# Performance work log

Measured on AMD Instinct MI355X. Metric: run time of the kernel, lower is better.

Reference implementation:

```python
import jax, jax.numpy as jnp
import numpy as np

V, H, B, NS, SL, QL, AL = 100000, 256, 64, 40, 30, 20, 12
NUM_EPISODE = 3


def setup_inputs() -> dict:
    key = jax.random.key(0)
    ks = iter(jax.random.split(key, 48))
    def p(shape, scale=0.05):
        return jax.random.normal(next(ks), shape, jnp.float32) * scale
    d = {}
    d["c_p"] = jax.random.randint(next(ks), (B, NS, SL), 0, V, dtype=jnp.int32)
    d["c_mask"] = jnp.zeros((B, NS, SL), jnp.int32)
    d["q_p"] = jax.random.randint(next(ks), (B, QL), 0, V, dtype=jnp.int32)
    d["q_mask"] = jnp.zeros((B, QL), jnp.int32)
    d["a_I_p"] = jax.random.randint(next(ks), (B, AL), 0, V, dtype=jnp.int32)
    d["a_I_mask"] = jnp.zeros((B, AL), jnp.int32)
    d["a_II_p"] = jax.random.randint(next(ks), (B, AL), 0, V, dtype=jnp.int32)
    d["a_II_mask"] = jnp.zeros((B, AL), jnp.int32)
    d["embed"] = p((V, H)).at[0].set(0.0)  # padding_idx=0
    for name in ["ctx", "q", "ans", "attn", "mem"]:
        d[name + "_Wih"] = p((3 * H, H))
        d[name + "_Whh"] = p((3 * H, H))
        d[name + "_bih"] = p((3 * H,))
        d[name + "_bhh"] = p((3 * H,))
    d["gate_W1"] = p((H, 7 * H)); d["gate_b1"] = p((H,))
    d["gate_W2"] = p((1, H));     d["gate_b2"] = p((1,))
    d["out_W1"] = p((H, 3 * H)); d["out_b1"] = p((H,))
    d["out_W2"] = p((2, H));     d["out_b2"] = p((2,))
    return d


def _gru_step(h, gi_t, Whh, bhh):
    # PyTorch GRU cell math; gates ordered (r, z, n)
    gh = h @ Whh.T + bhh
    i_r, i_z, i_n = jnp.split(gi_t, 3, -1)
    h_r, h_z, h_n = jnp.split(gh, 3, -1)
    r = jax.nn.sigmoid(i_r + h_r)
    z = jax.nn.sigmoid(i_z + h_z)
    n = jnp.tanh(i_n + r * h_n)
    return (1.0 - z) * n + z * h


def _run_gru(x, Wih, Whh, bih, bhh):
    # x: [N, T, H] -> outputs [N, T, H], zero initial hidden
    gi = jnp.einsum('nth,gh->ntg', x, Wih) + bih  # precompute input projections
    h0 = jnp.zeros((x.shape[0], Whh.shape[1]), x.dtype)
    def step(h, g_t):
        h2 = _gru_step(h, g_t, Whh, bhh)
        return h2, h2
    _, outs = jax.lax.scan(step, h0, jnp.swapaxes(gi, 0, 1))
    return jnp.swapaxes(outs, 0, 1)


def _gather_last(outs, mask):
    # real_length = number of zeros in mask (0 marks a valid token)
    lengths = jnp.sum(mask == 0, axis=-1)
    idx = jnp.clip(lengths - 1, 0, outs.shape[1] - 1)
    return jnp.take_along_axis(outs, idx[:, None, None], axis=1)[:, 0]


def _forward(c_p, c_mask, q_p, q_mask, a_I_p, a_I_mask, a_II_p, a_II_mask,
             embed,
             ctx_Wih, ctx_Whh, ctx_bih, ctx_bhh,
             q_Wih, q_Whh, q_bih, q_bhh,
             ans_Wih, ans_Whh, ans_bih, ans_bhh,
             attn_Wih, attn_Whh, attn_bih, attn_bhh,
             mem_Wih, mem_Whh, mem_bih, mem_bhh,
             gate_W1, gate_b1, gate_W2, gate_b2,
             out_W1, out_b1, out_W2, out_b2):
    b, ns, sl = c_p.shape
    # Context encoding: all (batch, sentence) pairs through one batched GRU
    ce = embed[c_p.reshape(b * ns, sl)]                      # [B*NS, SL, H]
    c_out = _run_gru(ce, ctx_Wih, ctx_Whh, ctx_bih, ctx_bhh)
    enc_ctx = _gather_last(c_out, c_mask.reshape(b * ns, sl)).reshape(b, ns, -1)  # [B, NS, H]
    # Question / answers
    enc_q = _gather_last(_run_gru(embed[q_p], q_Wih, q_Whh, q_bih, q_bhh), q_mask)          # [B, H]
    enc_a1 = _gather_last(_run_gru(embed[a_I_p], ans_Wih, ans_Whh, ans_bih, ans_bhh), a_I_mask)
    enc_a2 = _gather_last(_run_gru(embed[a_II_p], ans_Wih, ans_Whh, ans_bih, ans_bhh), a_II_mask)
    # Episodic memory: gated attention GRU scan over context sentences
    ctx_t = jnp.swapaxes(enc_ctx, 0, 1)  # [NS, B, H]
    memory = enc_q
    for _ in range(NUM_EPISODE):
        mem_now = memory
        def step(h, ct):
            feat = jnp.concatenate([ct, mem_now, enc_q, ct * enc_q, ct * mem_now,
                                    jnp.abs(ct - enc_q), jnp.abs(ct - mem_now)], axis=1)  # [B, 7H]
            g = jax.nn.sigmoid(jnp.tanh(feat @ gate_W1.T + gate_b1) @ gate_W2.T + gate_b2)  # [B, 1]
            hc = _gru_step(h, ct @ attn_Wih.T + attn_bih, attn_Whh, attn_bhh)
            return g * hc + (1.0 - g) * h, None
        e, _ = jax.lax.scan(step, jnp.zeros_like(memory), ctx_t)
        memory = _gru_step(memory, e @ mem_Wih.T + mem_bih, mem_Whh, mem_bhh)
    final = jnp.concatenate([memory, enc_a1, enc_a2], axis=1)  # [B, 3H]
    logits = jnp.tanh(final @ out_W1.T + out_b1) @ out_W2.T + out_b2  # [B, 2]
    return jax.nn.softmax(logits, axis=-1)


def reference(c_p, c_mask, q_p, q_mask, a_I_p, a_I_mask, a_II_p, a_II_mask,
              embed,
              ctx_Wih, ctx_Whh, ctx_bih, ctx_bhh,
              q_Wih, q_Whh, q_bih, q_bhh,
              ans_Wih, ans_Whh, ans_bih, ans_bhh,
              attn_Wih, attn_Whh, attn_bih, attn_bhh,
              mem_Wih, mem_Whh, mem_bih, mem_bhh,
              gate_W1, gate_b1, gate_W2, gate_b2,
              out_W1, out_b1, out_W2, out_b2):
    return _forward(c_p, c_mask, q_p, q_mask, a_I_p, a_I_mask, a_II_p, a_II_mask,
                    embed,
                    ctx_Wih, ctx_Whh, ctx_bih, ctx_bhh,
                    q_Wih, q_Whh, q_bih, q_bhh,
                    ans_Wih, ans_Whh, ans_bih, ans_bhh,
                    attn_Wih, attn_Whh, attn_bih, attn_bhh,
                    mem_Wih, mem_Whh, mem_bih, mem_bhh,
                    gate_W1, gate_b1, gate_W2, gate_b2,
                    out_W1, out_b1, out_W2, out_b2)
```

## Files before the change

kernel.cpp:

```cpp
#include <hip/hip_runtime.h>

typedef unsigned short u16;
typedef __bf16 bf16x8 __attribute__((ext_vector_type(8)));
typedef float f32x4 __attribute__((ext_vector_type(4)));

#define NSENT 40
#define SLEN 30
#define QLEN 20
#define ALEN 12
#define SCTX 2560

__device__ __forceinline__ float b2f(u16 u){ union{float f; unsigned i;} v; v.i = ((unsigned)u)<<16; return v.f; }
__device__ __forceinline__ u16 f2b(float f){ union{float f; unsigned u;} v; v.f=f; unsigned u=v.u; u += ((u>>16)&1u) + 0x7fffu; return (u16)(u>>16); }
__device__ __forceinline__ float sigm(float x){ return __builtin_amdgcn_rcpf(1.f + __expf(-x)); }
__device__ __forceinline__ float tanh_(float x){
  float a = fminf(fmaxf(2.f*x, -30.f), 30.f);
  float e = __expf(a);
  return 1.f - 2.f*__builtin_amdgcn_rcpf(e + 1.f);
}
__device__ __forceinline__ f32x4 mfma16(bf16x8 a, bf16x8 b, f32x4 c){
  return __builtin_amdgcn_mfma_f32_16x16x32_bf16(a, b, c, 0, 0, 0);
}

__global__ void k_prep(
    const float* s0,const float* s1,const float* s2,const float* s3,const float* s4,
    const float* s5,const float* s6,const float* s7,const float* s8,const float* s9,
    const float* s10,
    u16* d0,u16* d1,u16* d2,u16* d3,u16* d4,u16* d5,u16* d6,u16* d7,u16* d8,u16* d9,u16* d10)
{
  int i = blockIdx.x*512 + threadIdx.x;
  const float* s; u16* d; int off;
  if (i < 1966080){
    int seg = i/196608; off = i - seg*196608;
    switch(seg){
      case 0: s=s0; d=d0; break;  case 1: s=s1; d=d1; break;
      case 2: s=s2; d=d2; break;  case 3: s=s3; d=d3; break;
      case 4: s=s4; d=d4; break;  case 5: s=s5; d=d5; break;
      case 6: s=s6; d=d6; break;  case 7: s=s7; d=d7; break;
      case 8: s=s8; d=d8; break;  default: s=s9; d=d9; break;
    }
  } else { s=s10; d=d10; off = i - 1966080; }
  d[off] = f2b(s[off]);
}

__global__ __launch_bounds__(512, 2) void k_xproj(
    const int* c_p, const int* q_p, const int* a1p, const int* a2p,
    const float* embed,
    const u16* cWihB, const u16* qWihB, const u16* aWihB,
    const float* cbih, const float* qbih, const float* abih,
    u16* gi_c, u16* gi_q, u16* gi_a1, u16* gi_a2)
{
  __shared__ u16 xb[32][264];
  __shared__ u16 go[32][776];
  int bid=blockIdx.x, tid=threadIdx.x;
  const int* toks; const u16* W; const float* bias; u16* out; int rl;
  if (bid < 2400){ toks=c_p; W=cWihB; bias=cbih; out=gi_c; rl=bid*32; }
  else if (bid < 2440){ toks=q_p; W=qWihB; bias=qbih; out=gi_q; rl=(bid-2400)*32; }
  else if (bid < 2464){ toks=a1p; W=aWihB; bias=abih; out=gi_a1; rl=(bid-2440)*32; }
  else               { toks=a2p; W=aWihB; bias=abih; out=gi_a2; rl=(bid-2464)*32; }
  #pragma unroll
  for (int p=0;p<4;p++){
    int i=p*512+tid; int row=i>>6, f4=i&63;
    int tok = toks[rl+row];
    float4 v = *((const float4*)(embed + (long)tok*256) + f4);
    u16* dst = &xb[row][f4*4];
    dst[0]=f2b(v.x); dst[1]=f2b(v.y); dst[2]=f2b(v.z); dst[3]=f2b(v.w);
  }
  const int w=tid>>6, lane=tid&63, c=lane&15, quad=lane>>4;
  f32x4 acc[2][6];
  #pragma unroll
  for (int Mt=0;Mt<2;Mt++)
    #pragma unroll
    for (int nt=0;nt<6;nt++) acc[Mt][nt]=(f32x4){0.f,0.f,0.f,0.f};
  __syncthreads();
  #pragma unroll
  for (int Kt=0;Kt<8;Kt++){
    bf16x8 a0 = *(const bf16x8*)&xb[c][Kt*32+quad*8];
    bf16x8 a1 = *(const bf16x8*)&xb[16+c][Kt*32+quad*8];
    #pragma unroll
    for (int nt=0;nt<6;nt++){
      bf16x8 bfr = *(const bf16x8*)(W + ((w*6+nt)*16+c)*256 + Kt*32 + quad*8);
      acc[0][nt]=mfma16(a0,bfr,acc[0][nt]);
      acc[1][nt]=mfma16(a1,bfr,acc[1][nt]);
    }
  }
  float biasv[6];
  #pragma unroll
  for (int nt=0;nt<6;nt++) biasv[nt]=bias[(w*6+nt)*16+c];
  #pragma unroll
  for (int Mt=0;Mt<2;Mt++)
    #pragma unroll
    for (int nt=0;nt<6;nt++)
      #pragma unroll
      for (int r=0;r<4;r++)
        go[Mt*16+quad*4+r][(w*6+nt)*16+c]=f2b(acc[Mt][nt][r]+biasv[nt]);
  __syncthreads();
  #pragma unroll
  for (int p=0;p<6;p++){
    int idx=p*512+tid;
    int row=idx/96, ch=idx-row*96;
    *(uint4*)(out + (long)(rl+row)*768 + ch*8) = *(uint4*)((char*)&go[row][0] + ch*16);
  }
}

__global__ __launch_bounds__(512, 2) void k_enc_scan(
    const int* c_mask, const int* q_mask, const int* a1m, const int* a2m,
    const u16* cWhhB, const u16* qWhhB, const u16* aWhhB,
    const float* cbhh, const float* qbhh, const float* abhh,
    const u16* gi_c, const u16* gi_q, const u16* gi_a1, const u16* gi_a2,
    u16* enc_hi, u16* enc_lo, float* enc_qf, float* enc_a1f, float* enc_a2f)
{
  __shared__ u16 hhi[16][264];
  __shared__ u16 hlo[16][264];
  __shared__ float gh[16][772];
  __shared__ float holdf[16][256];
  __shared__ float bhl[768];
  __shared__ int idxs[16];
  int bid=blockIdx.x, tid=threadIdx.x;
  const int* msk; const u16* W; const float* bhh; const u16* gi; int T, seq0, mode;
  u16 *ohi=0, *olo=0; float* of=0;
  if (bid<160){ msk=c_mask; W=cWhhB; bhh=cbhh; gi=gi_c; T=SLEN; seq0=bid*16; mode=0; ohi=enc_hi; olo=enc_lo; }
  else if (bid<164){ msk=q_mask; W=qWhhB; bhh=qbhh; gi=gi_q; T=QLEN; seq0=(bid-160)*16; mode=1; of=enc_qf; }
  else if (bid<168){ msk=a1m; W=aWhhB; bhh=abhh; gi=gi_a1; T=ALEN; seq0=(bid-164)*16; mode=1; of=enc_a1f; }
  else             { msk=a2m; W=aWhhB; bhh=abhh; gi=gi_a2; T=ALEN; seq0=(bid-168)*16; mode=1; of=enc_a2f; }
  if (tid<16){
    int len=0; const int* mr=msk+(seq0+tid)*T;
    for (int t=0;t<T;t++) len += (mr[t]==0);
    int id=len-1; if(id<0)id=0; if(id>T-1)id=T-1; idxs[tid]=id;
  }
  for (int i=tid;i<16*264;i+=512){ ((u16*)hhi)[i]=0; ((u16*)hlo)[i]=0; }
  for (int i=tid;i<16*256;i+=512) ((float*)holdf)[i]=0.f;
  for (int i=tid;i<768;i+=512) bhl[i]=bhh[i];
  const int w=tid>>6, lane=tid&63, c=lane&15, quad=lane>>4;
  uint4 breg[48];
  #pragma unroll
  for (int nt=0;nt<6;nt++)
    #pragma unroll
    for (int Kt=0;Kt<8;Kt++)
      breg[nt*8+Kt] = *(const uint4*)(W + ((w*6+nt)*16+c)*256 + Kt*32 + quad*8);
  __syncthreads();

  for (int t=0;t<T;t++){
    f32x4 acc[6];
    #pragma unroll
    for (int nt=0;nt<6;nt++) acc[nt]=(f32x4){0.f,0.f,0.f,0.f};
    #pragma unroll
    for (int Kt=0;Kt<8;Kt++){
      bf16x8 a=*(const bf16x8*)&hhi[c][Kt*32+quad*8];
      #pragma unroll
      for (int nt=0;nt<6;nt++) acc[nt]=mfma16(a,*(const bf16x8*)&breg[nt*8+Kt],acc[nt]);
    }
    #pragma unroll
    for (int Kt=0;Kt<8;Kt++){
      bf16x8 a=*(const bf16x8*)&hlo[c][Kt*32+quad*8];
      #pragma unroll
      for (int nt=0;nt<6;nt++) acc[nt]=mfma16(a,*(const bf16x8*)&breg[nt*8+Kt],acc[nt]);
    }
    #pragma unroll
    for (int nt=0;nt<6;nt++)
      #pragma unroll
      for (int r=0;r<4;r++)
        gh[quad*4+r][(w*6+nt)*16+c]=acc[nt][r];
    __syncthreads();
    #pragma unroll
    for (int p=0;p<8;p++){
      int uid=p*512+tid; int m=uid>>8, j=uid&255;
      long grow=(long)(seq0+m)*T+t;
      const u16* gr = gi + grow*768;
      float ir=b2f(gr[j]), iz=b2f(gr[256+j]), in_=b2f(gr[512+j]);
      float hr=gh[m][j]+bhl[j], hz=gh[m][256+j]+bhl[256+j], hn=gh[m][512+j]+bhl[512+j];
      float rr=sigm(ir+hr), zz=sigm(iz+hz);
      float nn=tanh_(in_+rr*hn);
      float ho=holdf[m][j];
      float hnew=(1.f-zz)*nn+zz*ho;
      holdf[m][j]=hnew;
      u16 hi=f2b(hnew); float lof=hnew-b2f(hi); u16 lo=f2b(lof);
      hhi[m][j]=hi; hlo[m][j]=lo;
      if (t==idxs[m]){
        long o=(long)(seq0+m)*256+j;
        if (mode==0){ ohi[o]=hi; olo[o]=lo; }
        else of[o]=hnew;
      }
    }
    __syncthreads();
  }
}

__global__ __launch_bounds__(512, 2) void k_gi(
    const u16* enc_hi, const u16* enc_lo, const u16* tWihB, const float* tbih,
    float* gi_attn, const float* enc_qf, float* mem_f)
{
  int bid=blockIdx.x, tid=threadIdx.x;
  if (bid==40){ for (int i=tid;i<64*256;i+=512) mem_f[i]=enc_qf[i]; return; }
  __shared__ u16 ahi[64][264];
  __shared__ u16 alo[64][264];
  int seq0=bid*64;
  #pragma unroll
  for (int p=0;p<4;p++){
    int i=p*512+tid; int row=i>>5, ch=i&31;
    *(uint4*)((char*)&ahi[row][0]+ch*16) = *((const uint4*)(enc_hi+(long)(seq0+row)*256)+ch);
    *(uint4*)((char*)&alo[row][0]+ch*16) = *((const uint4*)(enc_lo+(long)(seq0+row)*256)+ch);
  }
  const int w=tid>>6, lane=tid&63, c=lane&15, quad=lane>>4;
  f32x4 acc[4][6];
  #pragma unroll
  for (int Mt=0;Mt<4;Mt++)
    #pragma unroll
    for (int nt=0;nt<6;nt++) acc[Mt][nt]=(f32x4){0.f,0.f,0.f,0.f};
  __syncthreads();
  #pragma unroll
  for (int Kt=0;Kt<8;Kt++){
    bf16x8 a[4];
    #pragma unroll
    for (int Mt=0;Mt<4;Mt++) a[Mt]=*(const bf16x8*)&ahi[Mt*16+c][Kt*32+quad*8];
    #pragma unroll
    for (int nt=0;nt<6;nt++){
      bf16x8 bfr=*(const bf16x8*)(tWihB + ((w*6+nt)*16+c)*256 + Kt*32 + quad*8);
      #pragma unroll
      for (int Mt=0;Mt<4;Mt++) acc[Mt][nt]=mfma16(a[Mt],bfr,acc[Mt][nt]);
    }
  }
  #pragma unroll
  for (int Kt=0;Kt<8;Kt++){
    bf16x8 a[4];
    #pragma unroll
    for (int Mt=0;Mt<4;Mt++) a[Mt]=*(const bf16x8*)&alo[Mt*16+c][Kt*32+quad*8];
    #pragma unroll
    for (int nt=0;nt<6;nt++){
      bf16x8 bfr=*(const bf16x8*)(tWihB + ((w*6+nt)*16+c)*256 + Kt*32 + quad*8);
      #pragma unroll
      for (int Mt=0;Mt<4;Mt++) acc[Mt][nt]=mfma16(a[Mt],bfr,acc[Mt][nt]);
    }
  }
  #pragma unroll
  for (int nt=0;nt<6;nt++){
    float bv=tbih[(w*6+nt)*16+c];
    #pragma unroll
    for (int Mt=0;Mt<4;Mt++)
      #pragma unroll
      for (int r=0;r<4;r++)
        gi_attn[(long)(seq0+Mt*16+quad*4+r)*768 + (w*6+nt)*16+c] = acc[Mt][nt][r]+bv;
  }
}

__global__ __launch_bounds__(512, 1) void k_gate(
    const u16* enc_hi, const u16* enc_lo, const float* mem_f, const float* enc_qf,
    const u16* W1, const float* b1, const float* W2, const float* b2, float* g)
{
  __shared__ float ctf[32][257];
  __shared__ float mvf[32][257];
  __shared__ float qvf[32][257];
  __shared__ u16 ab[32][264];
  __shared__ float pl[32][8];
  int bid=blockIdx.x, tid=threadIdx.x, seq0=bid*32;
  #pragma unroll
  for (int p=0;p<16;p++){
    int i=p*512+tid; int row=i>>8, j=i&255;
    int grow=seq0+row; int b=grow/NSENT;
    ctf[row][j]=b2f(enc_hi[(long)grow*256+j])+b2f(enc_lo[(long)grow*256+j]);
    mvf[row][j]=mem_f[b*256+j];
    qvf[row][j]=enc_qf[b*256+j];
  }
  const int w=tid>>6, lane=tid&63, c=lane&15, quad=lane>>4;
  f32x4 acc[2][2];
  float w2v[2];
  #pragma unroll
  for (int nt=0;nt<2;nt++){
    int n=(w*2+nt)*16+c;
    float bv=b1[n];
    acc[0][nt]=(f32x4){bv,bv,bv,bv}; acc[1][nt]=acc[0][nt];
    w2v[nt]=W2[n];
  }
  for (int ch=0; ch<7; ch++){
    __syncthreads();
    #pragma unroll
    for (int p=0;p<16;p++){
      int i=p*512+tid; int row=i>>8, j=i&255;
      float ct=ctf[row][j], mv=mvf[row][j], qv=qvf[row][j];
      float v;
      if      (ch==0) v=ct;
      else if (ch==1) v=mv;
      else if (ch==2) v=qv;
      else if (ch==3) v=ct*qv;
      else if (ch==4) v=ct*mv;
      else if (ch==5) v=fabsf(ct-qv);
      else            v=fabsf(ct-mv);
      ab[row][j]=f2b(v);
    }
    __syncthreads();
    #pragma unroll
    for (int Kt=0;Kt<8;Kt++){
      bf16x8 a0=*(const bf16x8*)&ab[c][Kt*32+quad*8];
      bf16x8 a1=*(const bf16x8*)&ab[16+c][Kt*32+quad*8];
      #pragma unroll
      for (int nt=0;nt<2;nt++){
        int n=(w*2+nt)*16+c;
        bf16x8 bfr=*(const bf16x8*)(W1 + (long)n*1792 + ch*256 + Kt*32 + quad*8);
        acc[0][nt]=mfma16(a0,bfr,acc[0][nt]);
        acc[1][nt]=mfma16(a1,bfr,acc[1][nt]);
      }
    }
  }
  float pm[8];
  #pragma unroll
  for (int i=0;i<8;i++){
    int Mt=i>>2, r=i&3;
    float s=0.f;
    #pragma unroll
    for (int nt=0;nt<2;nt++) s += tanh_(acc[Mt][nt][r])*w2v[nt];
    pm[i]=s;
  }
  #pragma unroll
  for (int off=1;off<16;off<<=1)
    #pragma unroll
    for (int i=0;i<8;i++) pm[i]+=__shfl_xor(pm[i],off,64);
  if (c==0){
    #pragma unroll
    for (int i=0;i<8;i++){ int m=(i>>2)*16+quad*4+(i&3); pl[m][w]=pm[i]; }
  }
  __syncthreads();
  if (tid<32){
    float s=b2[0];
    #pragma unroll
    for (int ww=0;ww<8;ww++) s+=pl[tid][ww];
    g[seq0+tid]=sigm(s);
  }
}

__global__ __launch_bounds__(512, 2) void k_scan(
    const u16* tWhhB, const float* tbhh,
    const float* gi_attn, const float* g,
    float* mem_f, const u16* mWihB, const u16* mWhhB,
    const float* mbih, const float* mbhh)
{
  __shared__ u16 hb[16][264];
  __shared__ u16 mhi[16][264];
  __shared__ u16 mlo[16][264];
  __shared__ float gh[4][772];
  __shared__ float gh2[4][772];
  __shared__ float holdf[4][256];
  __shared__ float memfl[4][256];
  __shared__ float bhl[768];
  int bid=blockIdx.x, tid=threadIdx.x, b0=bid*4;
  const int w=tid>>6, lane=tid&63, c=lane&15, quad=lane>>4;
  for (int i=tid;i<16*264;i+=512){ ((u16*)hb)[i]=0; ((u16*)mhi)[i]=0; ((u16*)mlo)[i]=0; }
  for (int i=tid;i<1024;i+=512){
    int m=i>>8, j=i&255;
    holdf[m][j]=0.f;
    float v=mem_f[(b0+m)*256+j]; memfl[m][j]=v;
    u16 hi=f2b(v); mhi[m][j]=hi; mlo[m][j]=f2b(v-b2f(hi));
  }
  for (int i=tid;i<768;i+=512) bhl[i]=tbhh[i];
  uint4 breg[48];
  #pragma unroll
  for (int nt=0;nt<6;nt++)
    #pragma unroll
    for (int Kt=0;Kt<8;Kt++)
      breg[nt*8+Kt] = *(const uint4*)(tWhhB + ((w*6+nt)*16+c)*256 + Kt*32 + quad*8);
  __syncthreads();

  for (int s=0;s<NSENT;s++){
    f32x4 acc[6];
    #pragma unroll
    for (int nt=0;nt<6;nt++) acc[nt]=(f32x4){0.f,0.f,0.f,0.f};
    #pragma unroll
    for (int Kt=0;Kt<8;Kt++){
      bf16x8 a=*(const bf16x8*)&hb[c][Kt*32+quad*8];
      #pragma unroll
      for (int nt=0;nt<6;nt++) acc[nt]=mfma16(a,*(const bf16x8*)&breg[nt*8+Kt],acc[nt]);
    }
    if (quad==0){
      #pragma unroll
      for (int nt=0;nt<6;nt++)
        #pragma unroll
        for (int r=0;r<4;r++)
          gh[r][(w*6+nt)*16+c]=acc[nt][r];
    }
    __syncthreads();
    #pragma unroll
    for (int p=0;p<2;p++){
      int uid=p*512+tid; int m=uid>>8, j=uid&255;
      int row=(b0+m)*NSENT+s;
      float gv=g[row];
      const float* gr=gi_attn+(long)row*768;
      float ir=gr[j], iz=gr[256+j], in_=gr[512+j];
      float hr=gh[m][j]+bhl[j], hz=gh[m][256+j]+bhl[256+j], hn=gh[m][512+j]+bhl[512+j];
      float rr=sigm(ir+hr), zz=sigm(iz+hz), nn=tanh_(in_+rr*hn);
      float ho=holdf[m][j];
      float hc=(1.f-zz)*nn+zz*ho;
      float hnew=gv*hc+(1.f-gv)*ho;
      holdf[m][j]=hnew;
      hb[m][j]=f2b(hnew);
    }
    __syncthreads();
  }
  f32x4 ai[6], ah[6];
  #pragma unroll
  for (int nt=0;nt<6;nt++){ ai[nt]=(f32x4){0.f,0.f,0.f,0.f}; ah[nt]=ai[nt]; }
  #pragma unroll
  for (int Kt=0;Kt<8;Kt++){
    bf16x8 a=*(const bf16x8*)&hb[c][Kt*32+quad*8];
    #pragma unroll
    for (int nt=0;nt<6;nt++){
      bf16x8 bfr=*(const bf16x8*)(mWihB + ((w*6+nt)*16+c)*256 + Kt*32 + quad*8);
      ai[nt]=mfma16(a,bfr,ai[nt]);
    }
  }
  #pragma unroll
  for (int Kt=0;Kt<8;Kt++){
    bf16x8 a=*(const bf16x8*)&mhi[c][Kt*32+quad*8];
    #pragma unroll
    for (int nt=0;nt<6;nt++){
      bf16x8 bfr=*(const bf16x8*)(mWhhB + ((w*6+nt)*16+c)*256 + Kt*32 + quad*8);
      ah[nt]=mfma16(a,bfr,ah[nt]);
    }
  }
  #pragma unroll
  for (int Kt=0;Kt<8;Kt++){
    bf16x8 a=*(const bf16x8*)&mlo[c][Kt*32+quad*8];
    #pragma unroll
    for (int nt=0;nt<6;nt++){
      bf16x8 bfr=*(const bf16x8*)(mWhhB + ((w*6+nt)*16+c)*256 + Kt*32 + quad*8);
      ah[nt]=mfma16(a,bfr,ah[nt]);
    }
  }
  if (quad==0){
    #pragma unroll
    for (int nt=0;nt<6;nt++)
      #pragma unroll
      for (int r=0;r<4;r++){
        gh[r][(w*6+nt)*16+c]=ai[nt][r];
        gh2[r][(w*6+nt)*16+c]=ah[nt][r];
      }
  }
  __syncthreads();
  #pragma unroll
  for (int p=0;p<2;p++){
    int uid=p*512+tid; int m=uid>>8, j=uid&255;
    float ir=gh[m][j]+mbih[j], iz=gh[m][256+j]+mbih[256+j], in_=gh[m][512+j]+mbih[512+j];
    float hr=gh2[m][j]+mbhh[j], hz=gh2[m][256+j]+mbhh[256+j], hn=gh2[m][512+j]+mbhh[512+j];
    float rr=sigm(ir+hr), zz=sigm(iz+hz), nn=tanh_(in_+rr*hn);
    float mo=memfl[m][j];
    mem_f[(b0+m)*256+j]=(1.f-zz)*nn+zz*mo;
  }
}

__global__ void k_final(const float* mem_f, const float* a1f, const float* a2f,
    const float* W1o, const float* b1o, const float* W2o, const float* b2o, float* outp)
{
  __shared__ float af[768];
  __shared__ float tl[256];
  __shared__ float lg[2];
  int b=blockIdx.x, tid=threadIdx.x;
  af[tid]     = mem_f[b*256+tid];
  af[256+tid] = a1f[b*256+tid];
  af[512+tid] = a2f[b*256+tid];
  __syncthreads();
  float s=b1o[tid];
  const float* wr=W1o + (long)tid*768;
  for (int k=0;k<768;k++) s += af[k]*wr[k];
  tl[tid]=tanh_(s);
  __syncthreads();
  if (tid<2){
    float l=b2o[tid];
    const float* w2=W2o + tid*256;
    for (int k=0;k<256;k++) l += tl[k]*w2[k];
    lg[tid]=l;
  }
  __syncthreads();
  if (tid==0){
    float m=fmaxf(lg[0],lg[1]);
    float e0=__expf(lg[0]-m), e1=__expf(lg[1]-m);
    float inv=1.f/(e0+e1);
    outp[b*2]=e0*inv; outp[b*2+1]=e1*inv;
  }
}

extern "C" void kernel_launch(void* const* d_in, const int* in_sizes, int n_in,
                              void* d_out, int out_size, void* d_ws, size_t ws_size,
                              hipStream_t stream) {
  const int* c_p   = (const int*)d_in[0];
  const int* c_m   = (const int*)d_in[1];
  const int* q_p   = (const int*)d_in[2];
  const int* q_m   = (const int*)d_in[3];
  const int* a1p   = (const int*)d_in[4];
  const int* a1m   = (const int*)d_in[5];
  const int* a2p   = (const int*)d_in[6];
  const int* a2m   = (const int*)d_in[7];
  const float* embed = (const float*)d_in[8];
  const float* cWih=(const float*)d_in[9],  *cWhh=(const float*)d_in[10], *cbih=(const float*)d_in[11], *cbhh=(const float*)d_in[12];
  const float* qWih=(const float*)d_in[13], *qWhh=(const float*)d_in[14], *qbih=(const float*)d_in[15], *qbhh=(const float*)d_in[16];
  const float* aWih=(const float*)d_in[17], *aWhh=(const float*)d_in[18], *abih=(const float*)d_in[19], *abhh=(const float*)d_in[20];
  const float* tWih=(const float*)d_in[21], *tWhh=(const float*)d_in[22], *tbih=(const float*)d_in[23], *tbhh=(const float*)d_in[24];
  const float* mWih=(const float*)d_in[25], *mWhh=(const float*)d_in[26], *mbih=(const float*)d_in[27], *mbhh=(const float*)d_in[28];
  const float* gW1=(const float*)d_in[29], *gb1=(const float*)d_in[30], *gW2=(const float*)d_in[31], *gb2=(const float*)d_in[32];
  const float* oW1=(const float*)d_in[33], *ob1=(const float*)d_in[34], *oW2=(const float*)d_in[35], *ob2=(const float*)d_in[36];

  char* ws = (char*)d_ws;
  size_t off = 0;
  u16* cWihB=(u16*)(ws+off); off+=393216;
  u16* cWhhB=(u16*)(ws+off); off+=393216;
  u16* qWihB=(u16*)(ws+off); off+=393216;
  u16* qWhhB=(u16*)(ws+off); off+=393216;
  u16* aWihB=(u16*)(ws+off); off+=393216;
  u16* aWhhB=(u16*)(ws+off); off+=393216;
  u16* tWihB=(u16*)(ws+off); off+=393216;
  u16* tWhhB=(u16*)(ws+off); off+=393216;
  u16* mWihB=(u16*)(ws+off); off+=393216;
  u16* mWhhB=(u16*)(ws+off); off+=393216;
  u16* gW1B =(u16*)(ws+off); off+=917504;
  u16* gi_c =(u16*)(ws+off); off+=(size_t)76800*768*2;
  u16* gi_q =(u16*)(ws+off); off+=(size_t)1280*768*2;
  u16* gi_a1=(u16*)(ws+off); off+=(size_t)768*768*2;
  u16* gi_a2=(u16*)(ws+off); off+=(size_t)768*768*2;
  u16* enc_hi=(u16*)(ws+off); off+=(size_t)SCTX*256*2;
  u16* enc_lo=(u16*)(ws+off); off+=(size_t)SCTX*256*2;
  float* enc_qf =(float*)(ws+off); off+=64*256*4;
  float* enc_a1f=(float*)(ws+off); off+=64*256*4;
  float* enc_a2f=(float*)(ws+off); off+=64*256*4;
  float* mem_f  =(float*)(ws+off); off+=64*256*4;
  float* gi_attn=(float*)(ws+off); off+=(size_t)SCTX*768*4;
  float* gbuf   =(float*)(ws+off); off+=SCTX*4;

  k_prep<<<4736, 512, 0, stream>>>(cWih,cWhh,qWih,qWhh,aWih,aWhh,tWih,tWhh,mWih,mWhh,gW1,
      cWihB,cWhhB,qWihB,qWhhB,aWihB,aWhhB,tWihB,tWhhB,mWihB,mWhhB,gW1B);

  k_xproj<<<2488, 512, 0, stream>>>(c_p,q_p,a1p,a2p, embed,
      cWihB,qWihB,aWihB, cbih,qbih,abih, gi_c,gi_q,gi_a1,gi_a2);

  k_enc_scan<<<172, 512, 0, stream>>>(c_m,q_m,a1m,a2m,
      cWhhB,qWhhB,aWhhB, cbhh,qbhh,abhh, gi_c,gi_q,gi_a1,gi_a2,
      enc_hi,enc_lo, enc_qf,enc_a1f,enc_a2f);

  k_gi<<<41, 512, 0, stream>>>(enc_hi,enc_lo, tWihB, tbih, gi_attn, enc_qf, mem_f);

  for (int ep=0; ep<3; ep++){
    k_gate<<<80, 512, 0, stream>>>(enc_hi,enc_lo, mem_f, enc_qf, gW1B, gb1, gW2, gb2, gbuf);
    k_scan<<<16, 512, 0, stream>>>(tWhhB, tbhh, gi_attn, gbuf, mem_f, mWihB, mWhhB, mbih, mbhh);
  }

  k_final<<<64, 256, 0, stream>>>(mem_f, enc_a1f, enc_a2f, oW1, ob1, oW2, ob2, (float*)d_out);
}
```

Baseline: 1.046 ms.

## Permute GRU gate weights so gate math stays in registers, prefetch inputs

Weights and biases of the encoder and attention GRUs are reordered at prep time so each wave's MFMA output tiles hold matching r/z/n columns. The gate nonlinearities can then be computed straight from accumulators with the hidden state kept in registers, dropping the shared-memory gh round trip and one barrier per timestep. The next timestep's input projections are double-buffered into shared memory while the MFMAs run. The gate MLP is also split so the memory-independent chunks (ctx, q, ctx*q, |ctx-q|) are computed once before the episodes, leaving only three chunks per episode. The costs are more register pressure and an extra partial buffer, and the encoder's recurrent step is serial, so its latency is what matters.

```diff
diff --git a/kernel.cpp b/kernel.cpp
--- a/kernel.cpp
+++ b/kernel.cpp
@@ -23,41 +23,68 @@
 }
 
 __global__ void k_prep(
-    const float* s0,const float* s1,const float* s2,const float* s3,const float* s4,
-    const float* s5,const float* s6,const float* s7,const float* s8,const float* s9,
-    const float* s10,
-    u16* d0,u16* d1,u16* d2,u16* d3,u16* d4,u16* d5,u16* d6,u16* d7,u16* d8,u16* d9,u16* d10)
+    const float* cWih, const float* cWhh, const float* qWih, const float* qWhh,
+    const float* aWih, const float* aWhh, const float* tWih, const float* tWhh,
+    const float* mWih, const float* mWhh, const float* gW1,
+    const float* cbih, const float* cbhh, const float* qbih, const float* qbhh,
+    const float* abih, const float* abhh, const float* tbih, const float* tbhh,
+    u16* P0,u16* P1,u16* P2,u16* P3,u16* P4,u16* P5,u16* P6,u16* P7,
+    u16* PmWih, u16* PmWhh, u16* PgW1,
+    float* B0,float* B1,float* B2,float* B3,float* B4,float* B5,float* B6,float* B7)
 {
   int i = blockIdx.x*512 + threadIdx.x;
-  const float* s; u16* d; int off;
-  if (i < 1966080){
-    int seg = i/196608; off = i - seg*196608;
+  if (i < 1572864){
+    int seg = i/196608; int e = i - seg*196608;
+    int np = e>>8, k = e&255;
+    int g16 = np/48, rem = np - g16*48, gate = rem>>4, cc = rem&15;
+    int j = gate*256 + g16*16 + cc;
+    const float* S;
+    u16* D;
     switch(seg){
-      case 0: s=s0; d=d0; break;  case 1: s=s1; d=d1; break;
-      case 2: s=s2; d=d2; break;  case 3: s=s3; d=d3; break;
-      case 4: s=s4; d=d4; break;  case 5: s=s5; d=d5; break;
-      case 6: s=s6; d=d6; break;  case 7: s=s7; d=d7; break;
-      case 8: s=s8; d=d8; break;  default: s=s9; d=d9; break;
-    }
-  } else { s=s10; d=d10; off = i - 1966080; }
-  d[off] = f2b(s[off]);
+      case 0: S=cWih; D=P0; break; case 1: S=cWhh; D=P1; break;
+      case 2: S=qWih; D=P2; break; case 3: S=qWhh; D=P3; break;
+      case 4: S=aWih; D=P4; break; case 5: S=aWhh; D=P5; break;
+      case 6: S=tWih; D=P6; break; default: S=tWhh; D=P7; break;
+    }
+    D[e] = f2b(S[j*256 + k]);
+  } else if (i < 1966080){
+    int e = i - 1572864;
+    if (e < 196608) PmWih[e]=f2b(mWih[e]);
+    else PmWhh[e-196608]=f2b(mWhh[e-196608]);
+  } else if (i < 2424832){
+    int e = i - 1966080;
+    PgW1[e] = f2b(gW1[e]);
+  } else {
+    int e = i - 2424832;
+    int seg = e/768; int np = e - seg*768;
+    int g16 = np/48, rem = np - g16*48, gate = rem>>4, cc = rem&15;
+    int j = gate*256 + g16*16 + cc;
+    const float* S; float* D;
+    switch(seg){
+      case 0: S=cbih; D=B0; break; case 1: S=cbhh; D=B1; break;
+      case 2: S=qbih; D=B2; break; case 3: S=qbhh; D=B3; break;
+      case 4: S=abih; D=B4; break; case 5: S=abhh; D=B5; break;
+      case 6: S=tbih; D=B6; break; default: S=tbhh; D=B7; break;
+    }
+    D[np] = S[j];
+  }
 }
 
 __global__ __launch_bounds__(512, 2) void k_xproj(
     const int* c_p, const int* q_p, const int* a1p, const int* a2p,
     const float* embed,
-    const u16* cWihB, const u16* qWihB, const u16* aWihB,
-    const float* cbih, const float* qbih, const float* abih,
+    const u16* cWihP, const u16* qWihP, const u16* aWihP,
+    const float* cBih, const float* qBih, const float* aBih,
     u16* gi_c, u16* gi_q, u16* gi_a1, u16* gi_a2)
 {
   __shared__ u16 xb[32][264];
   __shared__ u16 go[32][776];
   int bid=blockIdx.x, tid=threadIdx.x;
   const int* toks; const u16* W; const float* bias; u16* out; int rl;
-  if (bid < 2400){ toks=c_p; W=cWihB; bias=cbih; out=gi_c; rl=bid*32; }
-  else if (bid < 2440){ toks=q_p; W=qWihB; bias=qbih; out=gi_q; rl=(bid-2400)*32; }
-  else if (bid < 2464){ toks=a1p; W=aWihB; bias=abih; out=gi_a1; rl=(bid-2440)*32; }
-  else               { toks=a2p; W=aWihB; bias=abih; out=gi_a2; rl=(bid-2464)*32; }
+  if (bid < 2400){ toks=c_p; W=cWihP; bias=cBih; out=gi_c; rl=bid*32; }
+  else if (bid < 2440){ toks=q_p; W=qWihP; bias=qBih; out=gi_q; rl=(bid-2400)*32; }
+  else if (bid < 2464){ toks=a1p; W=aWihP; bias=aBih; out=gi_a1; rl=(bid-2440)*32; }
+  else               { toks=a2p; W=aWihP; bias=aBih; out=gi_a2; rl=(bid-2464)*32; }
   #pragma unroll
   for (int p=0;p<4;p++){
     int i=p*512+tid; int row=i>>6, f4=i&63;
@@ -79,7 +106,9 @@
     bf16x8 a1 = *(const bf16x8*)&xb[16+c][Kt*32+quad*8];
     #pragma unroll
     for (int nt=0;nt<6;nt++){
-      bf16x8 bfr = *(const bf16x8*)(W + ((w*6+nt)*16+c)*256 + Kt*32 + quad*8);
+      bf16x8 bfr = *(const bf16x8*)(cWihP==W||qWihP==W||aWihP==W ?
+                    W + ((w*6+nt)*16+c)*256 + Kt*32 + quad*8 :
+                    W + ((w*6+nt)*16+c)*256 + Kt*32 + quad*8);
       acc[0][nt]=mfma16(a0,bfr,acc[0][nt]);
       acc[1][nt]=mfma16(a1,bfr,acc[1][nt]);
     }
@@ -105,42 +134,65 @@
 
 __global__ __launch_bounds__(512, 2) void k_enc_scan(
     const int* c_mask, const int* q_mask, const int* a1m, const int* a2m,
-    const u16* cWhhB, const u16* qWhhB, const u16* aWhhB,
-    const float* cbhh, const float* qbhh, const float* abhh,
+    const u16* cWhhP, const u16* qWhhP, const u16* aWhhP,
+    const float* cBhh, const float* qBhh, const float* aBhh,
     const u16* gi_c, const u16* gi_q, const u16* gi_a1, const u16* gi_a2,
     u16* enc_hi, u16* enc_lo, float* enc_qf, float* enc_a1f, float* enc_a2f)
 {
   __shared__ u16 hhi[16][264];
   __shared__ u16 hlo[16][264];
-  __shared__ float gh[16][772];
-  __shared__ float holdf[16][256];
-  __shared__ float bhl[768];
+  __shared__ u16 gib[2][16][768];
   __shared__ int idxs[16];
   int bid=blockIdx.x, tid=threadIdx.x;
   const int* msk; const u16* W; const float* bhh; const u16* gi; int T, seq0, mode;
   u16 *ohi=0, *olo=0; float* of=0;
-  if (bid<160){ msk=c_mask; W=cWhhB; bhh=cbhh; gi=gi_c; T=SLEN; seq0=bid*16; mode=0; ohi=enc_hi; olo=enc_lo; }
-  else if (bid<164){ msk=q_mask; W=qWhhB; bhh=qbhh; gi=gi_q; T=QLEN; seq0=(bid-160)*16; mode=1; of=enc_qf; }
-  else if (bid<168){ msk=a1m; W=aWhhB; bhh=abhh; gi=gi_a1; T=ALEN; seq0=(bid-164)*16; mode=1; of=enc_a1f; }
-  else             { msk=a2m; W=aWhhB; bhh=abhh; gi=gi_a2; T=ALEN; seq0=(bid-168)*16; mode=1; of=enc_a2f; }
+  if (bid<160){ msk=c_mask; W=cWhhP; bhh=cBhh; gi=gi_c; T=SLEN; seq0=bid*16; mode=0; ohi=enc_hi; olo=enc_lo; }
+  else if (bid<164){ msk=q_mask; W=qWhhP; bhh=qBhh; gi=gi_q; T=QLEN; seq0=(bid-160)*16; mode=1; of=enc_qf; }
+  else if (bid<168){ msk=a1m; W=aWhhP; bhh=aBhh; gi=gi_a1; T=ALEN; seq0=(bid-164)*16; mode=1; of=enc_a1f; }
+  else             { msk=a2m; W=aWhhP; bhh=aBhh; gi=gi_a2; T=ALEN; seq0=(bid-168)*16; mode=1; of=enc_a2f; }
   if (tid<16){
     int len=0; const int* mr=msk+(seq0+tid)*T;
     for (int t=0;t<T;t++) len += (mr[t]==0);
     int id=len-1; if(id<0)id=0; if(id>T-1)id=T-1; idxs[tid]=id;
   }
   for (int i=tid;i<16*264;i+=512){ ((u16*)hhi)[i]=0; ((u16*)hlo)[i]=0; }
-  for (int i=tid;i<16*256;i+=512) ((float*)holdf)[i]=0.f;
-  for (int i=tid;i<768;i+=512) bhl[i]=bhh[i];
   const int w=tid>>6, lane=tid&63, c=lane&15, quad=lane>>4;
+  float biasv[6];
+  #pragma unroll
+  for (int nt=0;nt<6;nt++) biasv[nt]=bhh[w*96+nt*16+c];
   uint4 breg[48];
   #pragma unroll
   for (int nt=0;nt<6;nt++)
     #pragma unroll
     for (int Kt=0;Kt<8;Kt++)
-      breg[nt*8+Kt] = *(const uint4*)(W + ((w*6+nt)*16+c)*256 + Kt*32 + quad*8);
-  __syncthreads();
-
+      breg[nt*8+Kt] = *(const uint4*)(W + (w*96+nt*16+c)*256 + Kt*32 + quad*8);
+  float hreg[8];
+  #pragma unroll
+  for (int i=0;i<8;i++) hreg[i]=0.f;
+  const u16* gp[3];
+  #pragma unroll
+  for (int p=0;p<3;p++){
+    int idx=p*512+tid; int row=idx/96, ch=idx-row*96;
+    gp[p] = gi + ((long)(seq0+row)*T)*768 + ch*8;
+  }
+  u16* gf0 = &gib[0][0][0];
+  u16* gf1 = &gib[1][0][0];
+  {
+    uint4 s0[3];
+    #pragma unroll
+    for (int p=0;p<3;p++) s0[p]=*(const uint4*)(gp[p]);
+    #pragma unroll
+    for (int p=0;p<3;p++) *(uint4*)(gf0 + (p*512+tid)*8) = s0[p];
+  }
+  __syncthreads();
+  int cbuf=0;
   for (int t=0;t<T;t++){
+    uint4 pre[3];
+    bool pf = (t+1<T);
+    if (pf){
+      #pragma unroll
+      for (int p=0;p<3;p++) pre[p]=*(const uint4*)(gp[p]+(long)(t+1)*768);
+    }
     f32x4 acc[6];
     #pragma unroll
     for (int nt=0;nt<6;nt++) acc[nt]=(f32x4){0.f,0.f,0.f,0.f};
@@ -156,38 +208,45 @@
       #pragma unroll
       for (int nt=0;nt<6;nt++) acc[nt]=mfma16(a,*(const bf16x8*)&breg[nt*8+Kt],acc[nt]);
     }
-    #pragma unroll
-    for (int nt=0;nt<6;nt++)
-      #pragma unroll
-      for (int r=0;r<4;r++)
-        gh[quad*4+r][(w*6+nt)*16+c]=acc[nt][r];
+    if (pf){
+      u16* gs = cbuf ? gf0 : gf1;
+      #pragma unroll
+      for (int p=0;p<3;p++) *(uint4*)(gs + (p*512+tid)*8) = pre[p];
+    }
+    const u16* gb = cbuf ? gf1 : gf0;
+    #pragma unroll
+    for (int r=0;r<4;r++){
+      int m = quad*4+r;
+      const u16* gr = gb + m*768 + w*96 + c;
+      #pragma unroll
+      for (int jj=0;jj<2;jj++){
+        int j = w*32+jj*16+c;
+        float ir = b2f(gr[jj*48]);
+        float iz = b2f(gr[jj*48+16]);
+        float in_= b2f(gr[jj*48+32]);
+        float hr = acc[jj*3+0][r]+biasv[jj*3+0];
+        float hz = acc[jj*3+1][r]+biasv[jj*3+1];
+        float hn = acc[jj*3+2][r]+biasv[jj*3+2];
+        float rr=sigm(ir+hr), zz=sigm(iz+hz), nn=tanh_(in_+rr*hn);
+        float ho=hreg[r*2+jj];
+        float hnew=(1.f-zz)*nn+zz*ho;
+        hreg[r*2+jj]=hnew;
+        u16 hi_=f2b(hnew); u16 lo_=f2b(hnew-b2f(hi_));
+        hhi[m][j]=hi_; hlo[m][j]=lo_;
+        if (t==idxs[m]){
+          long o=(long)(seq0+m)*256+j;
+          if (mode==0){ ohi[o]=hi_; olo[o]=lo_; }
+          else of[o]=hnew;
+        }
+      }
+    }
     __syncthreads();
-    #pragma unroll
-    for (int p=0;p<8;p++){
-      int uid=p*512+tid; int m=uid>>8, j=uid&255;
-      long grow=(long)(seq0+m)*T+t;
-      const u16* gr = gi + grow*768;
-      float ir=b2f(gr[j]), iz=b2f(gr[256+j]), in_=b2f(gr[512+j]);
-      float hr=gh[m][j]+bhl[j], hz=gh[m][256+j]+bhl[256+j], hn=gh[m][512+j]+bhl[512+j];
-      float rr=sigm(ir+hr), zz=sigm(iz+hz);
-      float nn=tanh_(in_+rr*hn);
-      float ho=holdf[m][j];
-      float hnew=(1.f-zz)*nn+zz*ho;
-      holdf[m][j]=hnew;
-      u16 hi=f2b(hnew); float lof=hnew-b2f(hi); u16 lo=f2b(lof);
-      hhi[m][j]=hi; hlo[m][j]=lo;
-      if (t==idxs[m]){
-        long o=(long)(seq0+m)*256+j;
-        if (mode==0){ ohi[o]=hi; olo[o]=lo; }
-        else of[o]=hnew;
-      }
-    }
-    __syncthreads();
+    cbuf^=1;
   }
 }
 
 __global__ __launch_bounds__(512, 2) void k_gi(
-    const u16* enc_hi, const u16* enc_lo, const u16* tWihB, const float* tbih,
+    const u16* enc_hi, const u16* enc_lo, const u16* tWihP, const float* tBih,
     float* gi_attn, const float* enc_qf, float* mem_f)
 {
   int bid=blockIdx.x, tid=threadIdx.x;
@@ -215,7 +274,7 @@
     for (int Mt=0;Mt<4;Mt++) a[Mt]=*(const bf16x8*)&ahi[Mt*16+c][Kt*32+quad*8];
     #pragma unroll
     for (int nt=0;nt<6;nt++){
-      bf16x8 bfr=*(const bf16x8*)(tWihB + ((w*6+nt)*16+c)*256 + Kt*32 + quad*8);
+      bf16x8 bfr=*(const bf16x8*)(tWihP + ((w*6+nt)*16+c)*256 + Kt*32 + quad*8);
       #pragma unroll
       for (int Mt=0;Mt<4;Mt++) acc[Mt][nt]=mfma16(a[Mt],bfr,acc[Mt][nt]);
     }
@@ -227,14 +286,14 @@
     for (int Mt=0;Mt<4;Mt++) a[Mt]=*(const bf16x8*)&alo[Mt*16+c][Kt*32+quad*8];
     #pragma unroll
     for (int nt=0;nt<6;nt++){
-      bf16x8 bfr=*(const bf16x8*)(tWihB + ((w*6+nt)*16+c)*256 + Kt*32 + quad*8);
+      bf16x8 bfr=*(const bf16x8*)(tWihP + ((w*6+nt)*16+c)*256 + Kt*32 + quad*8);
       #pragma unroll
       for (int Mt=0;Mt<4;Mt++) acc[Mt][nt]=mfma16(a[Mt],bfr,acc[Mt][nt]);
     }
   }
   #pragma unroll
   for (int nt=0;nt<6;nt++){
-    float bv=tbih[(w*6+nt)*16+c];
+    float bv=tBih[(w*6+nt)*16+c];
     #pragma unroll
     for (int Mt=0;Mt<4;Mt++)
       #pragma unroll
@@ -243,48 +302,41 @@
   }
 }
 
-__global__ __launch_bounds__(512, 1) void k_gate(
-    const u16* enc_hi, const u16* enc_lo, const float* mem_f, const float* enc_qf,
-    const u16* W1, const float* b1, const float* W2, const float* b2, float* g)
+__global__ __launch_bounds__(512, 1) void k_gatepre(
+    const u16* enc_hi, const u16* enc_lo, const float* enc_qf,
+    const u16* W1, const float* b1, float* partial)
 {
   __shared__ float ctf[32][257];
-  __shared__ float mvf[32][257];
   __shared__ float qvf[32][257];
   __shared__ u16 ab[32][264];
-  __shared__ float pl[32][8];
   int bid=blockIdx.x, tid=threadIdx.x, seq0=bid*32;
   #pragma unroll
   for (int p=0;p<16;p++){
     int i=p*512+tid; int row=i>>8, j=i&255;
     int grow=seq0+row; int b=grow/NSENT;
     ctf[row][j]=b2f(enc_hi[(long)grow*256+j])+b2f(enc_lo[(long)grow*256+j]);
-    mvf[row][j]=mem_f[b*256+j];
     qvf[row][j]=enc_qf[b*256+j];
   }
   const int w=tid>>6, lane=tid&63, c=lane&15, quad=lane>>4;
   f32x4 acc[2][2];
-  float w2v[2];
   #pragma unroll
   for (int nt=0;nt<2;nt++){
-    int n=(w*2+nt)*16+c;
-    float bv=b1[n];
+    float bv=b1[(w*2+nt)*16+c];
     acc[0][nt]=(f32x4){bv,bv,bv,bv}; acc[1][nt]=acc[0][nt];
-    w2v[nt]=W2[n];
-  }
-  for (int ch=0; ch<7; ch++){
+  }
+  const int chl[4]={0,2,3,5};
+  for (int ci=0; ci<4; ci++){
+    int ch=chl[ci];
     __syncthreads();
     #pragma unroll
     for (int p=0;p<16;p++){
       int i=p*512+tid; int row=i>>8, j=i&255;
-      float ct=ctf[row][j], mv=mvf[row][j], qv=qvf[row][j];
+      float ct=ctf[row][j], qv=qvf[row][j];
       float v;
       if      (ch==0) v=ct;
-      else if (ch==1) v=mv;
       else if (ch==2) v=qv;
       else if (ch==3) v=ct*qv;
-      else if (ch==4) v=ct*mv;
-      else if (ch==5) v=fabsf(ct-qv);
-      else            v=fabsf(ct-mv);
+      else            v=fabsf(ct-qv);
       ab[row][j]=f2b(v);
     }
     __syncthreads();
@@ -301,6 +353,72 @@
       }
     }
   }
+  #pragma unroll
+  for (int Mt=0;Mt<2;Mt++)
+    #pragma unroll
+    for (int nt=0;nt<2;nt++)
+      #pragma unroll
+      for (int r=0;r<4;r++)
+        partial[(long)(seq0+Mt*16+quad*4+r)*256 + (w*2+nt)*16+c] = acc[Mt][nt][r];
+}
+
+__global__ __launch_bounds__(512, 1) void k_gate(
+    const u16* enc_hi, const u16* enc_lo, const float* mem_f,
+    const float* partial, const u16* W1, const float* W2, const float* b2v, float* g)
+{
+  __shared__ float ctf[32][257];
+  __shared__ float mvf[32][257];
+  __shared__ u16 ab[32][264];
+  __shared__ float pl[32][8];
+  int bid=blockIdx.x, tid=threadIdx.x, seq0=bid*32;
+  #pragma unroll
+  for (int p=0;p<16;p++){
+    int i=p*512+tid; int row=i>>8, j=i&255;
+    int grow=seq0+row; int b=grow/NSENT;
+    ctf[row][j]=b2f(enc_hi[(long)grow*256+j])+b2f(enc_lo[(long)grow*256+j]);
+    mvf[row][j]=mem_f[b*256+j];
+  }
+  const int w=tid>>6, lane=tid&63, c=lane&15, quad=lane>>4;
+  f32x4 acc[2][2];
+  float w2v[2];
+  #pragma unroll
+  for (int nt=0;nt<2;nt++){
+    int n=(w*2+nt)*16+c;
+    w2v[nt]=W2[n];
+    #pragma unroll
+    for (int Mt=0;Mt<2;Mt++)
+      #pragma unroll
+      for (int r=0;r<4;r++)
+        acc[Mt][nt][r]=partial[(long)(seq0+Mt*16+quad*4+r)*256 + n];
+  }
+  const int chl[3]={1,4,6};
+  for (int ci=0; ci<3; ci++){
+    int ch=chl[ci];
+    __syncthreads();
+    #pragma unroll
+    for (int p=0;p<16;p++){
+      int i=p*512+tid; int row=i>>8, j=i&255;
+      float ct=ctf[row][j], mv=mvf[row][j];
+      float v;
+      if      (ch==1) v=mv;
+      else if (ch==4) v=ct*mv;
+      else            v=fabsf(ct-mv);
+      ab[row][j]=f2b(v);
+    }
+    __syncthreads();
+    #pragma unroll
+    for (int Kt=0;Kt<8;Kt++){
+      bf16x8 a0=*(const bf16x8*)&ab[c][Kt*32+quad*8];
+      bf16x8 a1=*(const bf16x8*)&ab[16+c][Kt*32+quad*8];
+      #pragma unroll
+      for (int nt=0;nt<2;nt++){
+        int n=(w*2+nt)*16+c;
+        bf16x8 bfr=*(const bf16x8*)(W1 + (long)n*1792 + ch*256 + Kt*32 + quad*8);
+        acc[0][nt]=mfma16(a0,bfr,acc[0][nt]);
+        acc[1][nt]=mfma16(a1,bfr,acc[1][nt]);
+      }
+    }
+  }
   float pm[8];
   #pragma unroll
   for (int i=0;i<8;i++){
@@ -320,7 +438,7 @@
   }
   __syncthreads();
   if (tid<32){
-    float s=b2[0];
+    float s=b2v[0];
     #pragma unroll
     for (int ww=0;ww<8;ww++) s+=pl[tid][ww];
     g[seq0+tid]=sigm(s);
@@ -328,7 +446,7 @@
 }
 
 __global__ __launch_bounds__(512, 2) void k_scan(
-    const u16* tWhhB, const float* tbhh,
+    const u16* tWhhP, const float* tBhh,
     const float* gi_attn, const float* g,
     float* mem_f, const u16* mWihB, const u16* mWhhB,
     const float* mbih, const float* mbhh)
@@ -336,30 +454,51 @@
   __shared__ u16 hb[16][264];
   __shared__ u16 mhi[16][264];
   __shared__ u16 mlo[16][264];
+  __shared__ float gia[2][3072];
+  __shared__ float gl[4][40];
   __shared__ float gh[4][772];
   __shared__ float gh2[4][772];
-  __shared__ float holdf[4][256];
   __shared__ float memfl[4][256];
-  __shared__ float bhl[768];
   int bid=blockIdx.x, tid=threadIdx.x, b0=bid*4;
   const int w=tid>>6, lane=tid&63, c=lane&15, quad=lane>>4;
   for (int i=tid;i<16*264;i+=512){ ((u16*)hb)[i]=0; ((u16*)mhi)[i]=0; ((u16*)mlo)[i]=0; }
   for (int i=tid;i<1024;i+=512){
     int m=i>>8, j=i&255;
-    holdf[m][j]=0.f;
     float v=mem_f[(b0+m)*256+j]; memfl[m][j]=v;
-    u16 hi=f2b(v); mhi[m][j]=hi; mlo[m][j]=f2b(v-b2f(hi));
-  }
-  for (int i=tid;i<768;i+=512) bhl[i]=tbhh[i];
+    u16 hi_=f2b(v); mhi[m][j]=hi_; mlo[m][j]=f2b(v-b2f(hi_));
+  }
+  if (tid<160){ int m=tid/40, s=tid-m*40; gl[m][s]=g[(b0+m)*40+s]; }
+  float biasv[6];
+  #pragma unroll
+  for (int nt=0;nt<6;nt++) biasv[nt]=tBhh[w*96+nt*16+c];
   uint4 breg[48];
   #pragma unroll
   for (int nt=0;nt<6;nt++)
     #pragma unroll
     for (int Kt=0;Kt<8;Kt++)
-      breg[nt*8+Kt] = *(const uint4*)(tWhhB + ((w*6+nt)*16+c)*256 + Kt*32 + quad*8);
-  __syncthreads();
-
+      breg[nt*8+Kt] = *(const uint4*)(tWhhP + (w*96+nt*16+c)*256 + Kt*32 + quad*8);
+  float hreg[8];
+  #pragma unroll
+  for (int i=0;i<8;i++) hreg[i]=0.f;
+  int i4a = tid, i4b = 512+tid;
+  int ma = i4a/192, ca=(i4a-ma*192)*4;
+  int mb = i4b/192, cb=(i4b-mb*192)*4;
+  const float* gpa = gi_attn + ((long)(b0+ma)*40)*768 + ca;
+  const float* gpb = gi_attn + ((long)(b0+mb)*40)*768 + cb;
+  {
+    float4 v0=*(const float4*)(gpa);
+    *(float4*)&gia[0][i4a*4]=v0;
+    if (tid<256){ float4 v1=*(const float4*)(gpb); *(float4*)&gia[0][i4b*4]=v1; }
+  }
+  __syncthreads();
+  int cbuf=0;
   for (int s=0;s<NSENT;s++){
+    float4 p0, p1;
+    bool pf=(s+1<NSENT);
+    if (pf){
+      p0=*(const float4*)(gpa + (long)(s+1)*768);
+      if (tid<256) p1=*(const float4*)(gpb + (long)(s+1)*768);
+    }
     f32x4 acc[6];
     #pragma unroll
     for (int nt=0;nt<6;nt++) acc[nt]=(f32x4){0.f,0.f,0.f,0.f};
@@ -369,30 +508,37 @@
       #pragma unroll
       for (int nt=0;nt<6;nt++) acc[nt]=mfma16(a,*(const bf16x8*)&breg[nt*8+Kt],acc[nt]);
     }
+    if (pf){
+      float* gs=&gia[1^cbuf][0];
+      *(float4*)(gs+i4a*4)=p0;
+      if (tid<256) *(float4*)(gs+i4b*4)=p1;
+    }
     if (quad==0){
-      #pragma unroll
-      for (int nt=0;nt<6;nt++)
+      const float* ga=&gia[cbuf][0];
+      #pragma unroll
+      for (int r=0;r<4;r++){
+        float gv = gl[r][s];
+        const float* gr = ga + r*768 + w*96 + c;
         #pragma unroll
-        for (int r=0;r<4;r++)
-          gh[r][(w*6+nt)*16+c]=acc[nt][r];
+        for (int jj=0;jj<2;jj++){
+          int j = w*32+jj*16+c;
+          float ir = gr[jj*48];
+          float iz = gr[jj*48+16];
+          float in_= gr[jj*48+32];
+          float hr = acc[jj*3+0][r]+biasv[jj*3+0];
+          float hz = acc[jj*3+1][r]+biasv[jj*3+1];
+          float hn = acc[jj*3+2][r]+biasv[jj*3+2];
+          float rr=sigm(ir+hr), zz=sigm(iz+hz), nn=tanh_(in_+rr*hn);
+          float ho=hreg[r*2+jj];
+          float hc=(1.f-zz)*nn+zz*ho;
+          float hnew=gv*hc+(1.f-gv)*ho;
+          hreg[r*2+jj]=hnew;
+          hb[r][j]=f2b(hnew);
+        }
+      }
     }
     __syncthreads();
-    #pragma unroll
-    for (int p=0;p<2;p++){
-      int uid=p*512+tid; int m=uid>>8, j=uid&255;
-      int row=(b0+m)*NSENT+s;
-      float gv=g[row];
-      const float* gr=gi_attn+(long)row*768;
-      float ir=gr[j], iz=gr[256+j], in_=gr[512+j];
-      float hr=gh[m][j]+bhl[j], hz=gh[m][256+j]+bhl[256+j], hn=gh[m][512+j]+bhl[512+j];
-      float rr=sigm(ir+hr), zz=sigm(iz+hz), nn=tanh_(in_+rr*hn);
-      float ho=holdf[m][j];
-      float hc=(1.f-zz)*nn+zz*ho;
-      float hnew=gv*hc+(1.f-gv)*ho;
-      holdf[m][j]=hnew;
-      hb[m][j]=f2b(hnew);
-    }
-    __syncthreads();
+    cbuf^=1;
   }
   f32x4 ai[6], ah[6];
   #pragma unroll
@@ -498,17 +644,25 @@
 
   char* ws = (char*)d_ws;
   size_t off = 0;
-  u16* cWihB=(u16*)(ws+off); off+=393216;
-  u16* cWhhB=(u16*)(ws+off); off+=393216;
-  u16* qWihB=(u16*)(ws+off); off+=393216;
-  u16* qWhhB=(u16*)(ws+off); off+=393216;
-  u16* aWihB=(u16*)(ws+off); off+=393216;
-  u16* aWhhB=(u16*)(ws+off); off+=393216;
-  u16* tWihB=(u16*)(ws+off); off+=393216;
-  u16* tWhhB=(u16*)(ws+off); off+=393216;
-  u16* mWihB=(u16*)(ws+off); off+=393216;
-  u16* mWhhB=(u16*)(ws+off); off+=393216;
-  u16* gW1B =(u16*)(ws+off); off+=917504;
+  u16* P0=(u16*)(ws+off); off+=393216;
+  u16* P1=(u16*)(ws+off); off+=393216;
+  u16* P2=(u16*)(ws+off); off+=393216;
+  u16* P3=(u16*)(ws+off); off+=393216;
+  u16* P4=(u16*)(ws+off); off+=393216;
+  u16* P5=(u16*)(ws+off); off+=393216;
+  u16* P6=(u16*)(ws+off); off+=393216;
+  u16* P7=(u16*)(ws+off); off+=393216;
+  u16* PmWih=(u16*)(ws+off); off+=393216;
+  u16* PmWhh=(u16*)(ws+off); off+=393216;
+  u16* PgW1 =(u16*)(ws+off); off+=917504;
+  float* B0=(float*)(ws+off); off+=3072;
+  float* B1=(float*)(ws+off); off+=3072;
+  float* B2=(float*)(ws+off); off+=3072;
+  float* B3=(float*)(ws+off); off+=3072;
+  float* B4=(float*)(ws+off); off+=3072;
+  float* B5=(float*)(ws+off); off+=3072;
+  float* B6=(float*)(ws+off); off+=3072;
+  float* B7=(float*)(ws+off); off+=3072;
   u16* gi_c =(u16*)(ws+off); off+=(size_t)76800*768*2;
   u16* gi_q =(u16*)(ws+off); off+=(size_t)1280*768*2;
   u16* gi_a1=(u16*)(ws+off); off+=(size_t)768*768*2;
@@ -520,23 +674,28 @@
   float* enc_a2f=(float*)(ws+off); off+=64*256*4;
   float* mem_f  =(float*)(ws+off); off+=64*256*4;
   float* gi_attn=(float*)(ws+off); off+=(size_t)SCTX*768*4;
+  float* partial=(float*)(ws+off); off+=(size_t)SCTX*256*4;
   float* gbuf   =(float*)(ws+off); off+=SCTX*4;
 
-  k_prep<<<4736, 512, 0, stream>>>(cWih,cWhh,qWih,qWhh,aWih,aWhh,tWih,tWhh,mWih,mWhh,gW1,
-      cWihB,cWhhB,qWihB,qWhhB,aWihB,aWhhB,tWihB,tWhhB,mWihB,mWhhB,gW1B);
+  k_prep<<<4748, 512, 0, stream>>>(cWih,cWhh,qWih,qWhh,aWih,aWhh,tWih,tWhh,mWih,mWhh,gW1,
+      cbih,cbhh,qbih,qbhh,abih,abhh,tbih,tbhh,
+      P0,P1,P2,P3,P4,P5,P6,P7, PmWih,PmWhh,PgW1,
+      B0,B1,B2,B3,B4,B5,B6,B7);
 
   k_xproj<<<2488, 512, 0, stream>>>(c_p,q_p,a1p,a2p, embed,
-      cWihB,qWihB,aWihB, cbih,qbih,abih, gi_c,gi_q,gi_a1,gi_a2);
+      P0,P2,P4, B0,B2,B4, gi_c,gi_q,gi_a1,gi_a2);
 
   k_enc_scan<<<172, 512, 0, stream>>>(c_m,q_m,a1m,a2m,
-      cWhhB,qWhhB,aWhhB, cbhh,qbhh,abhh, gi_c,gi_q,gi_a1,gi_a2,
+      P1,P3,P5, B1,B3,B5, gi_c,gi_q,gi_a1,gi_a2,
       enc_hi,enc_lo, enc_qf,enc_a1f,enc_a2f);
 
-  k_gi<<<41, 512, 0, stream>>>(enc_hi,enc_lo, tWihB, tbih, gi_attn, enc_qf, mem_f);
+  k_gi<<<41, 512, 0, stream>>>(enc_hi,enc_lo, P6, B6, gi_attn, enc_qf, mem_f);
+
+  k_gatepre<<<80, 512, 0, stream>>>(enc_hi,enc_lo, enc_qf, PgW1, gb1, partial);
 
   for (int ep=0; ep<3; ep++){
-    k_gate<<<80, 512, 0, stream>>>(enc_hi,enc_lo, mem_f, enc_qf, gW1B, gb1, gW2, gb2, gbuf);
-    k_scan<<<16, 512, 0, stream>>>(tWhhB, tbhh, gi_attn, gbuf, mem_f, mWihB, mWhhB, mbih, mbhh);
+    k_gate<<<80, 512, 0, stream>>>(enc_hi,enc_lo, mem_f, partial, PgW1, gW2, gb2, gbuf);
+    k_scan<<<16, 512, 0, stream>>>(P7, B7, gi_attn, gbuf, mem_f, PmWih, PmWhh, mbih, mbhh);
   }
 
   k_final<<<64, 256, 0, stream>>>(mem_f, enc_a1f, enc_a2f, oW1, ob1, oW2, ob2, (float*)d_out);
```

Measured after the change: 957.7 us. 1.09x faster.
